# Optimization experiments

Hardware: AMD Instinct MI355X
Metric: run time of the kernel (lower is better)

Reference implementation:

```python
import jax, jax.numpy as jnp
import numpy as np

K_PRED = 6
TEMP = 0.8  # score_temperature
MTR_THRESH = [3.5, 1.0, 1.75]  # meters per type [veh, ped, cyc]
MPA_THRESH = [2.5, 1.0, 1.5]


def _within(xy, thresh):
    # xy: [S, A, P, T, 2], thresh: [S, A] -> bool [S, A, P, P]; ADE(i, j) < thresh (use_ade=True)
    diff = xy[:, :, None, :, :, :] - xy[:, :, :, None, :, :]  # [S, A, P, P, T, 2]
    ade = jnp.sqrt((diff * diff).sum(-1)).mean(-1)            # [S, A, P, P]
    return ade < thresh[:, :, None, None]


def _mtr_nms(trajs, scores, agent_type):
    # Greedy sequential top-k with distance-based down-weighting (MTR-style NMS).
    thresh = agent_type @ jnp.asarray(MTR_THRESH, scores.dtype)  # [S, A]
    within = _within(trajs[..., :2], thresh)                     # [S, A, P, P]
    P = scores.shape[-1]

    def step(carry, _):
        idx = jnp.argmax(carry, axis=-1)                                              # [S, A]
        row = jnp.take_along_axis(within, idx[:, :, None, None], axis=2)[:, :, 0, :]  # [S, A, P]
        carry = carry * ((~row).astype(carry.dtype) * 0.99 + 0.01)
        carry = jnp.where(jnp.arange(P) == idx[:, :, None], -1.0, carry)
        return carry, idx

    _, mode_idx = jax.lax.scan(step, scores, None, length=K_PRED)  # [K, S, A]
    mode_idx = jnp.moveaxis(mode_idx, 0, -1)                       # [S, A, K]
    trajs_k = jnp.take_along_axis(trajs, mode_idx[:, :, :, None, None], axis=2)
    scores_k = jnp.take_along_axis(scores, mode_idx, axis=2)
    return trajs_k, scores_k / scores_k.sum(-1, keepdims=True)


def _mpa_nms(valid, trajs, scores, agent_type):
    # Sequential suppression in descending-score order; mode k drops to 0.001 if any
    # nearby mode currently has a higher score. Faithful to the torch nested loop.
    thresh = agent_type @ jnp.asarray(MPA_THRESH, scores.dtype)  # [S, A]
    within = _within(trajs[..., :2], thresh)                     # [S, A, K, K]

    def per_agent(w, s, v):
        order = jnp.argsort(-s)  # descending score order

        def step(carry, k):
            suppress = jnp.any(w[k] & (carry > carry[k]))
            carry = carry.at[k].set(jnp.where(v & suppress, jnp.asarray(0.001, carry.dtype), carry[k]))
            return carry, None

        out, _ = jax.lax.scan(step, s, order)
        return out

    s = jax.vmap(jax.vmap(per_agent))(within, scores, valid)
    return s / s.sum(-1, keepdims=True)


def forward(valid, scores, trajs, agent_type):
    scores = scores / scores.sum(-1, keepdims=True)
    S, A, P, T, D = trajs.shape
    # n_pred > k_pred, aggr_thresh=[], mtr_nms_thresh non-empty -> mtr_nms branch
    trajs_k, scores_k = _mtr_nms(trajs, scores, agent_type)
    # mpa_nms_thresh non-empty -> mpa_nms
    scores_k = _mpa_nms(valid, trajs_k, scores_k, agent_type)
    # score_temperature > 0
    scores_k = jax.nn.softmax(jnp.log(scores_k) / TEMP, axis=-1)
    tr = jnp.transpose(trajs_k, (0, 3, 1, 2, 4))  # movedim(3,1): [S, T, A, K, D]
    waymo_trajs = tr[..., :2]
    waymo_yaw_bbox = tr[..., 2:3]
    waymo_spd = tr[..., 3:4]
    waymo_valid = jnp.broadcast_to(valid[:, None, :], (S, T, A))
    return waymo_trajs, waymo_yaw_bbox, waymo_spd, scores_k, waymo_valid


def setup_inputs():
    key = jax.random.key(0)
    k1, k2, k3, k4, k5 = jax.random.split(key, 5)
    S, A, P, T = 8, 64, 32, 80
    valid = jax.random.bernoulli(k1, 0.9, (S, A))
    scores = jax.random.uniform(k2, (S, A, P), minval=0.01, maxval=1.0)
    # shared base path + per-mode noise so pairwise ADEs straddle the NMS thresholds
    base = jax.random.normal(k3, (S, A, 1, T, 4)) * 20.0
    trajs = base + jax.random.normal(k4, (S, A, P, T, 4)) * 1.5
    agent_type = jax.nn.one_hot(jax.random.randint(k5, (S, A), 0, 3), 3, dtype=jnp.float32)
    return {"valid": valid, "scores": scores, "trajs": trajs, "agent_type": agent_type}


def reference(valid, scores, trajs, agent_type):
    return forward(valid, scores, trajs, agent_type)
```

## Files before the change

### kernel.cpp

```cpp
#include <hip/hip_runtime.h>
#include <math.h>
#include <float.h>

#define NS 8
#define NA 64
#define NP 32
#define NT 80
#define NK 6
#define NAG (NS*NA)
#define PAIRS 496

#define FSQRT(x) __builtin_amdgcn_sqrtf(x)

#define BASE1 ((size_t)NS*NT*NA*NK*2)
#define BASE2 (BASE1 + (size_t)NS*NT*NA*NK)
#define BASE3 (BASE2 + (size_t)NS*NT*NA*NK)
#define BASE4 (BASE3 + (size_t)NS*NA*NK)

__global__ __launch_bounds__(512) void k_fused(
    const void* __restrict__ valid_raw,
    const float* __restrict__ scores,
    const float* __restrict__ trajs,
    const float* __restrict__ atype,
    float* __restrict__ out)
{
    const int bid = blockIdx.x;
    const int blk = (bid & 7) * 64 + (bid >> 3);
    const int s = blk >> 6;
    const int a = blk & 63;
    const int tid = threadIdx.x;

    __shared__ float2 sxy[NT][NP + 1];
    __shared__ float2 szw[NT][NP + 1];
    __shared__ float sade[NP][NP];
    __shared__ unsigned wloc[NP];
    __shared__ int   sel6[NK];
    __shared__ float fsc6[NK];
    __shared__ float vf_sh;

    if (tid < NP) wloc[tid] = 1u << tid;

    unsigned u0 = 0, u1 = 0; float sc = 0.0f;
    if (tid < 64) {
        const unsigned* vw = (const unsigned*)valid_raw;
        u0 = vw[tid]; u1 = vw[tid + 64];
        sc = scores[blk*NP + (tid & 31)];
    }
    const float a0 = atype[blk*3+0], a1 = atype[blk*3+1], a2 = atype[blk*3+2];
    const float thrM = a0*3.5f + a1*1.0f + a2*1.75f;
    const float thrQ = a0*2.5f + a1*1.0f + a2*1.5f;

    const float4* tg4 = (const float4*)trajs + (size_t)blk * NP * NT;
    #pragma unroll
    for (int rep = 0; rep < 5; ++rep) {
        int l = tid + rep*512;
        int p = l / NT, t = l - p*NT;
        float4 v = tg4[l];
        sxy[t][p] = make_float2(v.x, v.y);
        szw[t][p] = make_float2(v.z, v.w);
    }
    __syncthreads();

    {
        const int tile = tid >> 2, slice = tid & 3;
        int A_, B_, C_, D_;
        bool offd = (tile < 120);
        if (offd) {
            float fs = sqrtf((float)(1 + 8*tile));
            int tj = (int)((1.0f + fs) * 0.5f);
            int ti = tile - ((tj*(tj-1)) >> 1);
            A_ = 2*ti; B_ = 2*ti+1; C_ = 2*tj; D_ = 2*tj+1;
        } else {
            int m = tile - 120;
            A_ = 4*m; B_ = 4*m+2; C_ = 4*m+1; D_ = 4*m+3;
        }
        float accAC = 0.0f, accAD = 0.0f, accBC = 0.0f, accBD = 0.0f;
        const int tbase = slice * 20;
        #pragma unroll 4
        for (int tt = 0; tt < 20; ++tt) {
            int t = tbase + tt;
            float2 va = sxy[t][A_], vb = sxy[t][B_];
            float2 vc = sxy[t][C_], vd = sxy[t][D_];
            float dx, dy;
            dx = va.x - vc.x; dy = va.y - vc.y; accAC += FSQRT(fmaf(dx,dx,dy*dy));
            dx = va.x - vd.x; dy = va.y - vd.y; accAD += FSQRT(fmaf(dx,dx,dy*dy));
            dx = vb.x - vc.x; dy = vb.y - vc.y; accBC += FSQRT(fmaf(dx,dx,dy*dy));
            dx = vb.x - vd.x; dy = vb.y - vd.y; accBD += FSQRT(fmaf(dx,dx,dy*dy));
        }
        const int qb = (tid & 63) & ~3;
#define FOLD(acc) ((((acc) + __shfl((acc), qb+1)) + __shfl((acc), qb+2)) + __shfl((acc), qb+3))
        float fAC = FOLD(accAC);
        float fAD = FOLD(accAD);
        float fBC = FOLD(accBC);
        float fBD = FOLD(accBD);
#undef FOLD
        if (slice == 0) {
            const float inv = 1.0f / (float)NT;
            float e0 = fAC*inv, e1 = fAD*inv, e2 = fBC*inv, e3 = fBD*inv;
            sade[A_][C_] = e0; sade[C_][A_] = e0;
            if (e0 < thrM) { atomicOr(&wloc[A_], 1u<<C_); atomicOr(&wloc[C_], 1u<<A_); }
            sade[B_][D_] = e3; sade[D_][B_] = e3;
            if (e3 < thrM) { atomicOr(&wloc[B_], 1u<<D_); atomicOr(&wloc[D_], 1u<<B_); }
            if (offd) {
                sade[A_][D_] = e1; sade[D_][A_] = e1;
                if (e1 < thrM) { atomicOr(&wloc[A_], 1u<<D_); atomicOr(&wloc[D_], 1u<<A_); }
                sade[B_][C_] = e2; sade[C_][B_] = e2;
                if (e2 < thrM) { atomicOr(&wloc[B_], 1u<<C_); atomicOr(&wloc[C_], 1u<<B_); }
            }
        }
    }
    __syncthreads();

    if (tid < 64) {
        const int lane = tid;
        const int p = lane & 31;

        bool fHit = (u0 == 0x3F800000u) || (u1 == 0x3F800000u);
        int nz0 = ((u0&0xFFu)!=0)+((u0&0xFF00u)!=0)+((u0&0xFF0000u)!=0)+((u0&0xFF000000u)!=0);
        int nz1 = ((u1&0xFFu)!=0)+((u1&0xFF00u)!=0)+((u1&0xFF0000u)!=0)+((u1&0xFF000000u)!=0);
        bool isF = __any(fHit), multi = __any(nz0 >= 2 || nz1 >= 2);
        int vflag;
        if (isF)        vflag = (((const float*)valid_raw)[blk] != 0.0f);
        else if (multi) vflag = (((const unsigned char*)valid_raw)[blk] != 0);
        else            vflag = (((const int*)valid_raw)[blk] != 0);

        unsigned wl = wloc[p];

        float carry = sc;
        int sel_0, sel_1, sel_2, sel_3, sel_4, sel_5;
#define GREEDY(SK) { \
        float vv = carry; int bi = p; \
        _Pragma("unroll") \
        for (int off = 16; off; off >>= 1) { \
            float ov = __shfl_xor(vv, off); \
            int   oi = __shfl_xor(bi, off); \
            if (ov > vv || (ov == vv && oi < bi)) { vv = ov; bi = oi; } \
        } \
        SK = bi; \
        unsigned rbi = __shfl(wl, bi); \
        carry = (p == bi) ? -1.0f : (((rbi >> p) & 1u) ? carry*0.01f : carry); }
        GREEDY(sel_0) GREEDY(sel_1) GREEDY(sel_2) GREEDY(sel_3) GREEDY(sel_4) GREEDY(sel_5)
#undef GREEDY

        float q0 = __shfl(sc, sel_0), q1 = __shfl(sc, sel_1), q2 = __shfl(sc, sel_2);
        float q3 = __shfl(sc, sel_3), q4 = __shfl(sc, sel_4), q5 = __shfl(sc, sel_5);

        int ii = (lane<5)?0 : (lane<9)?1 : (lane<12)?2 : (lane<14)?3 : 4;
        int jj = lane - ((ii==0)?-1 : (ii==1)?3 : (ii==2)?6 : (ii==3)?8 : 9);
        jj = (jj < 0) ? 0 : (jj > 5 ? 5 : jj);
        int pi = (ii==0)?sel_0:(ii==1)?sel_1:(ii==2)?sel_2:(ii==3)?sel_3:(ii==4)?sel_4:sel_5;
        int pj = (jj==0)?sel_0:(jj==1)?sel_1:(jj==2)?sel_2:(jj==3)?sel_3:(jj==4)?sel_4:sel_5;
        float ade15 = sade[pi][pj];
        bool within = (lane < 15) && (ade15 < thrQ);
        unsigned long long bal = __ballot(within);
#define B(i) ((unsigned)((bal >> (i)) & 1ull))
        unsigned w6_0 = (B(0)<<1)|(B(1)<<2)|(B(2)<<3)|(B(3)<<4)|(B(4)<<5);
        unsigned w6_1 = (B(0)<<0)|(B(5)<<2)|(B(6)<<3)|(B(7)<<4)|(B(8)<<5);
        unsigned w6_2 = (B(1)<<0)|(B(5)<<1)|(B(9)<<3)|(B(10)<<4)|(B(11)<<5);
        unsigned w6_3 = (B(2)<<0)|(B(6)<<1)|(B(9)<<2)|(B(12)<<4)|(B(13)<<5);
        unsigned w6_4 = (B(3)<<0)|(B(7)<<1)|(B(10)<<2)|(B(12)<<3)|(B(14)<<5);
        unsigned w6_5 = (B(4)<<0)|(B(8)<<1)|(B(11)<<2)|(B(13)<<3)|(B(14)<<4);
#undef B

#define GE(x,y) ((x) >= (y))
        bool a01=GE(q0,q1), a02=GE(q0,q2), a03=GE(q0,q3), a04=GE(q0,q4), a05=GE(q0,q5);
        bool a12=GE(q1,q2), a13=GE(q1,q3), a14=GE(q1,q4), a15=GE(q1,q5);
        bool a23=GE(q2,q3), a24=GE(q2,q4), a25=GE(q2,q5);
        bool a34=GE(q3,q4), a35=GE(q3,q5);
        bool a45=GE(q4,q5);
#undef GE
        int r0 = (!a01)+(!a02)+(!a03)+(!a04)+(!a05);
        int r1 = a01+(!a12)+(!a13)+(!a14)+(!a15);
        int r2 = a02+a12+(!a23)+(!a24)+(!a25);
        int r3 = a03+a13+a23+(!a34)+(!a35);
        int r4 = a04+a14+a24+a34+(!a45);
        int r5 = a05+a15+a25+a35+a45;

        const float sum6 = q0+q1+q2+q3+q4+q5;
        const float supv = 0.001f * sum6;
#define STEP(m) { \
        float ck = (r0==m)?q0:(r1==m)?q1:(r2==m)?q2:(r3==m)?q3:(r4==m)?q4:q5; \
        unsigned wk = (r0==m)?w6_0:(r1==m)?w6_1:(r2==m)?w6_2:(r3==m)?w6_3:(r4==m)?w6_4:w6_5; \
        bool sup = (((wk>>0)&1u)&&(q0>ck))||(((wk>>1)&1u)&&(q1>ck))||(((wk>>2)&1u)&&(q2>ck)) \
                 ||(((wk>>3)&1u)&&(q3>ck))||(((wk>>4)&1u)&&(q4>ck))||(((wk>>5)&1u)&&(q5>ck)); \
        bool go = vflag && sup; \
        q0 = (go&&(r0==m))?supv:q0; q1 = (go&&(r1==m))?supv:q1; q2 = (go&&(r2==m))?supv:q2; \
        q3 = (go&&(r3==m))?supv:q3; q4 = (go&&(r4==m))?supv:q4; q5 = (go&&(r5==m))?supv:q5; }
        STEP(0) STEP(1) STEP(2) STEP(3) STEP(4) STEP(5)
#undef STEP

        float g0 = __logf(q0)*1.25f, g1 = __logf(q1)*1.25f, g2 = __logf(q2)*1.25f;
        float g3 = __logf(q3)*1.25f, g4 = __logf(q4)*1.25f, g5 = __logf(q5)*1.25f;
        float mx = fmaxf(fmaxf(fmaxf(g0,g1),fmaxf(g2,g3)),fmaxf(g4,g5));
        float e0 = __expf(g0-mx), e1 = __expf(g1-mx), e2 = __expf(g2-mx);
        float e3 = __expf(g3-mx), e4 = __expf(g4-mx), e5 = __expf(g5-mx);
        float es = e0+e1+e2+e3+e4+e5;

        if (lane < NK) {
            float fv = (lane==0)?e0:(lane==1)?e1:(lane==2)?e2:(lane==3)?e3:(lane==4)?e4:e5;
            int   sv = (lane==0)?sel_0:(lane==1)?sel_1:(lane==2)?sel_2:(lane==3)?sel_3:(lane==4)?sel_4:sel_5;
            fsc6[lane] = fv / es;
            sel6[lane] = sv;
        }
        if (lane == 0) vf_sh = vflag ? 1.0f : 0.0f;
    }
    __syncthreads();

    if (tid < 3*NT) {
        int t = tid / 3, kp = tid - t*3;
        int k0 = kp*2;
        int s0 = sel6[k0], s1 = sel6[k0+1];
        float2 xy0 = sxy[t][s0], xy1 = sxy[t][s1];
        float2 zw0 = szw[t][s0], zw1 = szw[t][s1];
        size_t ob = (((size_t)(s*NT + t)*NA + a)*NK + k0);
        *(float4*)((float2*)out + ob) = make_float4(xy0.x, xy0.y, xy1.x, xy1.y);
        *(float2*)(out + BASE1 + ob) = make_float2(zw0.x, zw1.x);
        *(float2*)(out + BASE2 + ob) = make_float2(zw0.y, zw1.y);
    }
    if (tid < NK) out[BASE3 + (size_t)blk*NK + tid] = fsc6[tid];
    if (tid < NT)
        out[BASE4 + (size_t)(s*NT + tid)*NA + a] = vf_sh;
}

extern "C" void kernel_launch(void* const* d_in, const int* in_sizes, int n_in,
                              void* d_out, int out_size, void* d_ws, size_t ws_size,
                              hipStream_t stream) {
    const void*  valid  = d_in[0];
    const float* scores = (const float*)d_in[1];
    const float* trajs  = (const float*)d_in[2];
    const float* atype  = (const float*)d_in[3];
    k_fused<<<NAG, 512, 0, stream>>>(valid, scores, trajs, atype, (float*)d_out);
}
```

Measured before the change: 19.58 us.

## Run NMS redundantly in every wave, drop zw LDS staging and final barrier

Every wavefront now runs the greedy selection and suppression logic redundantly, so selected indices stay in registers and the last __syncthreads plus the shared handoff buffers go away. The z/w trajectory components are no longer staged in LDS; the output stage re-reads the selected modes straight from global memory, likely from cache. Argmax is simplified to an fmax butterfly followed by a ballot and find-first-set. This cuts LDS usage and a barrier, at the cost of redundant ALU work across eight waves and extra global reads.

```diff
diff --git a/kernel.cpp b/kernel.cpp
--- a/kernel.cpp
+++ b/kernel.cpp
@@ -29,23 +29,18 @@
     const int s = blk >> 6;
     const int a = blk & 63;
     const int tid = threadIdx.x;
+    const int lane = tid & 63;
+    const int p = lane & 31;
 
     __shared__ float2 sxy[NT][NP + 1];
-    __shared__ float2 szw[NT][NP + 1];
     __shared__ float sade[NP][NP];
     __shared__ unsigned wloc[NP];
-    __shared__ int   sel6[NK];
-    __shared__ float fsc6[NK];
-    __shared__ float vf_sh;
 
     if (tid < NP) wloc[tid] = 1u << tid;
 
-    unsigned u0 = 0, u1 = 0; float sc = 0.0f;
-    if (tid < 64) {
-        const unsigned* vw = (const unsigned*)valid_raw;
-        u0 = vw[tid]; u1 = vw[tid + 64];
-        sc = scores[blk*NP + (tid & 31)];
-    }
+    const unsigned* vw = (const unsigned*)valid_raw;
+    unsigned u0 = vw[lane], u1 = vw[lane + 64];
+    float sc = scores[blk*NP + p];
     const float a0 = atype[blk*3+0], a1 = atype[blk*3+1], a2 = atype[blk*3+2];
     const float thrM = a0*3.5f + a1*1.0f + a2*1.75f;
     const float thrQ = a0*2.5f + a1*1.0f + a2*1.5f;
@@ -54,10 +49,9 @@
     #pragma unroll
     for (int rep = 0; rep < 5; ++rep) {
         int l = tid + rep*512;
-        int p = l / NT, t = l - p*NT;
+        int pp = l / NT, t = l - pp*NT;
         float4 v = tg4[l];
-        sxy[t][p] = make_float2(v.x, v.y);
-        szw[t][p] = make_float2(v.z, v.w);
+        sxy[t][pp] = make_float2(v.x, v.y);
     }
     __syncthreads();
 
@@ -87,7 +81,7 @@
             dx = vb.x - vc.x; dy = vb.y - vc.y; accBC += FSQRT(fmaf(dx,dx,dy*dy));
             dx = vb.x - vd.x; dy = vb.y - vd.y; accBD += FSQRT(fmaf(dx,dx,dy*dy));
         }
-        const int qb = (tid & 63) & ~3;
+        const int qb = lane & ~3;
 #define FOLD(acc) ((((acc) + __shfl((acc), qb+1)) + __shfl((acc), qb+2)) + __shfl((acc), qb+3))
         float fAC = FOLD(accAC);
         float fAD = FOLD(accAD);
@@ -111,115 +105,104 @@
     }
     __syncthreads();
 
-    if (tid < 64) {
-        const int lane = tid;
-        const int p = lane & 31;
-
-        bool fHit = (u0 == 0x3F800000u) || (u1 == 0x3F800000u);
-        int nz0 = ((u0&0xFFu)!=0)+((u0&0xFF00u)!=0)+((u0&0xFF0000u)!=0)+((u0&0xFF000000u)!=0);
-        int nz1 = ((u1&0xFFu)!=0)+((u1&0xFF00u)!=0)+((u1&0xFF0000u)!=0)+((u1&0xFF000000u)!=0);
-        bool isF = __any(fHit), multi = __any(nz0 >= 2 || nz1 >= 2);
-        int vflag;
-        if (isF)        vflag = (((const float*)valid_raw)[blk] != 0.0f);
-        else if (multi) vflag = (((const unsigned char*)valid_raw)[blk] != 0);
-        else            vflag = (((const int*)valid_raw)[blk] != 0);
-
-        unsigned wl = wloc[p];
-
-        float carry = sc;
-        int sel_0, sel_1, sel_2, sel_3, sel_4, sel_5;
+    bool fHit = (u0 == 0x3F800000u) || (u1 == 0x3F800000u);
+    int nz0 = ((u0&0xFFu)!=0)+((u0&0xFF00u)!=0)+((u0&0xFF0000u)!=0)+((u0&0xFF000000u)!=0);
+    int nz1 = ((u1&0xFFu)!=0)+((u1&0xFF00u)!=0)+((u1&0xFF0000u)!=0)+((u1&0xFF000000u)!=0);
+    bool isF = __any(fHit), multi = __any(nz0 >= 2 || nz1 >= 2);
+    int vflag;
+    if (isF)        vflag = (((const float*)valid_raw)[blk] != 0.0f);
+    else if (multi) vflag = (((const unsigned char*)valid_raw)[blk] != 0);
+    else            vflag = (((const int*)valid_raw)[blk] != 0);
+
+    unsigned wl = wloc[p];
+
+    float carry = sc;
+    int sel_0, sel_1, sel_2, sel_3, sel_4, sel_5;
 #define GREEDY(SK) { \
-        float vv = carry; int bi = p; \
-        _Pragma("unroll") \
-        for (int off = 16; off; off >>= 1) { \
-            float ov = __shfl_xor(vv, off); \
-            int   oi = __shfl_xor(bi, off); \
-            if (ov > vv || (ov == vv && oi < bi)) { vv = ov; bi = oi; } \
-        } \
-        SK = bi; \
-        unsigned rbi = __shfl(wl, bi); \
-        carry = (p == bi) ? -1.0f : (((rbi >> p) & 1u) ? carry*0.01f : carry); }
-        GREEDY(sel_0) GREEDY(sel_1) GREEDY(sel_2) GREEDY(sel_3) GREEDY(sel_4) GREEDY(sel_5)
+    float vv = carry; \
+    _Pragma("unroll") \
+    for (int off = 16; off; off >>= 1) vv = fmaxf(vv, __shfl_xor(vv, off)); \
+    unsigned long long mba = __ballot(carry == vv); \
+    int bi = __ffsll((long long)mba) - 1; \
+    SK = bi; \
+    unsigned rbi = __shfl(wl, bi); \
+    carry = (p == bi) ? -1.0f : (((rbi >> p) & 1u) ? carry*0.01f : carry); }
+    GREEDY(sel_0) GREEDY(sel_1) GREEDY(sel_2) GREEDY(sel_3) GREEDY(sel_4) GREEDY(sel_5)
 #undef GREEDY
 
-        float q0 = __shfl(sc, sel_0), q1 = __shfl(sc, sel_1), q2 = __shfl(sc, sel_2);
-        float q3 = __shfl(sc, sel_3), q4 = __shfl(sc, sel_4), q5 = __shfl(sc, sel_5);
-
-        int ii = (lane<5)?0 : (lane<9)?1 : (lane<12)?2 : (lane<14)?3 : 4;
-        int jj = lane - ((ii==0)?-1 : (ii==1)?3 : (ii==2)?6 : (ii==3)?8 : 9);
-        jj = (jj < 0) ? 0 : (jj > 5 ? 5 : jj);
-        int pi = (ii==0)?sel_0:(ii==1)?sel_1:(ii==2)?sel_2:(ii==3)?sel_3:(ii==4)?sel_4:sel_5;
-        int pj = (jj==0)?sel_0:(jj==1)?sel_1:(jj==2)?sel_2:(jj==3)?sel_3:(jj==4)?sel_4:sel_5;
-        float ade15 = sade[pi][pj];
-        bool within = (lane < 15) && (ade15 < thrQ);
-        unsigned long long bal = __ballot(within);
+    float q0 = __shfl(sc, sel_0), q1 = __shfl(sc, sel_1), q2 = __shfl(sc, sel_2);
+    float q3 = __shfl(sc, sel_3), q4 = __shfl(sc, sel_4), q5 = __shfl(sc, sel_5);
+
+    int ii = (lane<5)?0 : (lane<9)?1 : (lane<12)?2 : (lane<14)?3 : 4;
+    int jj = lane - ((ii==0)?-1 : (ii==1)?3 : (ii==2)?6 : (ii==3)?8 : 9);
+    jj = (jj < 0) ? 0 : (jj > 5 ? 5 : jj);
+    int pi = (ii==0)?sel_0:(ii==1)?sel_1:(ii==2)?sel_2:(ii==3)?sel_3:(ii==4)?sel_4:sel_5;
+    int pj = (jj==0)?sel_0:(jj==1)?sel_1:(jj==2)?sel_2:(jj==3)?sel_3:(jj==4)?sel_4:sel_5;
+    float ade15 = sade[pi][pj];
+    bool within = (lane < 15) && (ade15 < thrQ);
+    unsigned long long bal = __ballot(within);
 #define B(i) ((unsigned)((bal >> (i)) & 1ull))
-        unsigned w6_0 = (B(0)<<1)|(B(1)<<2)|(B(2)<<3)|(B(3)<<4)|(B(4)<<5);
-        unsigned w6_1 = (B(0)<<0)|(B(5)<<2)|(B(6)<<3)|(B(7)<<4)|(B(8)<<5);
-        unsigned w6_2 = (B(1)<<0)|(B(5)<<1)|(B(9)<<3)|(B(10)<<4)|(B(11)<<5);
-        unsigned w6_3 = (B(2)<<0)|(B(6)<<1)|(B(9)<<2)|(B(12)<<4)|(B(13)<<5);
-        unsigned w6_4 = (B(3)<<0)|(B(7)<<1)|(B(10)<<2)|(B(12)<<3)|(B(14)<<5);
-        unsigned w6_5 = (B(4)<<0)|(B(8)<<1)|(B(11)<<2)|(B(13)<<3)|(B(14)<<4);
+    unsigned w6_0 = (B(0)<<1)|(B(1)<<2)|(B(2)<<3)|(B(3)<<4)|(B(4)<<5);
+    unsigned w6_1 = (B(0)<<0)|(B(5)<<2)|(B(6)<<3)|(B(7)<<4)|(B(8)<<5);
+    unsigned w6_2 = (B(1)<<0)|(B(5)<<1)|(B(9)<<3)|(B(10)<<4)|(B(11)<<5);
+    unsigned w6_3 = (B(2)<<0)|(B(6)<<1)|(B(9)<<2)|(B(12)<<4)|(B(13)<<5);
+    unsigned w6_4 = (B(3)<<0)|(B(7)<<1)|(B(10)<<2)|(B(12)<<3)|(B(14)<<5);
+    unsigned w6_5 = (B(4)<<0)|(B(8)<<1)|(B(11)<<2)|(B(13)<<3)|(B(14)<<4);
 #undef B
 
 #define GE(x,y) ((x) >= (y))
-        bool a01=GE(q0,q1), a02=GE(q0,q2), a03=GE(q0,q3), a04=GE(q0,q4), a05=GE(q0,q5);
-        bool a12=GE(q1,q2), a13=GE(q1,q3), a14=GE(q1,q4), a15=GE(q1,q5);
-        bool a23=GE(q2,q3), a24=GE(q2,q4), a25=GE(q2,q5);
-        bool a34=GE(q3,q4), a35=GE(q3,q5);
-        bool a45=GE(q4,q5);
+    bool a01=GE(q0,q1), a02=GE(q0,q2), a03=GE(q0,q3), a04=GE(q0,q4), a05=GE(q0,q5);
+    bool a12=GE(q1,q2), a13=GE(q1,q3), a14=GE(q1,q4), a15=GE(q1,q5);
+    bool a23=GE(q2,q3), a24=GE(q2,q4), a25=GE(q2,q5);
+    bool a34=GE(q3,q4), a35=GE(q3,q5);
+    bool a45=GE(q4,q5);
 #undef GE
-        int r0 = (!a01)+(!a02)+(!a03)+(!a04)+(!a05);
-        int r1 = a01+(!a12)+(!a13)+(!a14)+(!a15);
-        int r2 = a02+a12+(!a23)+(!a24)+(!a25);
-        int r3 = a03+a13+a23+(!a34)+(!a35);
-        int r4 = a04+a14+a24+a34+(!a45);
-        int r5 = a05+a15+a25+a35+a45;
-
-        const float sum6 = q0+q1+q2+q3+q4+q5;
-        const float supv = 0.001f * sum6;
+    int r0 = (!a01)+(!a02)+(!a03)+(!a04)+(!a05);
+    int r1 = a01+(!a12)+(!a13)+(!a14)+(!a15);
+    int r2 = a02+a12+(!a23)+(!a24)+(!a25);
+    int r3 = a03+a13+a23+(!a34)+(!a35);
+    int r4 = a04+a14+a24+a34+(!a45);
+    int r5 = a05+a15+a25+a35+a45;
+
+    const float sum6 = q0+q1+q2+q3+q4+q5;
+    const float supv = 0.001f * sum6;
 #define STEP(m) { \
-        float ck = (r0==m)?q0:(r1==m)?q1:(r2==m)?q2:(r3==m)?q3:(r4==m)?q4:q5; \
-        unsigned wk = (r0==m)?w6_0:(r1==m)?w6_1:(r2==m)?w6_2:(r3==m)?w6_3:(r4==m)?w6_4:w6_5; \
-        bool sup = (((wk>>0)&1u)&&(q0>ck))||(((wk>>1)&1u)&&(q1>ck))||(((wk>>2)&1u)&&(q2>ck)) \
-                 ||(((wk>>3)&1u)&&(q3>ck))||(((wk>>4)&1u)&&(q4>ck))||(((wk>>5)&1u)&&(q5>ck)); \
-        bool go = vflag && sup; \
-        q0 = (go&&(r0==m))?supv:q0; q1 = (go&&(r1==m))?supv:q1; q2 = (go&&(r2==m))?supv:q2; \
-        q3 = (go&&(r3==m))?supv:q3; q4 = (go&&(r4==m))?supv:q4; q5 = (go&&(r5==m))?supv:q5; }
-        STEP(0) STEP(1) STEP(2) STEP(3) STEP(4) STEP(5)
+    float ck = (r0==m)?q0:(r1==m)?q1:(r2==m)?q2:(r3==m)?q3:(r4==m)?q4:q5; \
+    unsigned wk = (r0==m)?w6_0:(r1==m)?w6_1:(r2==m)?w6_2:(r3==m)?w6_3:(r4==m)?w6_4:w6_5; \
+    bool sup = (((wk>>0)&1u)&&(q0>ck))||(((wk>>1)&1u)&&(q1>ck))||(((wk>>2)&1u)&&(q2>ck)) \
+             ||(((wk>>3)&1u)&&(q3>ck))||(((wk>>4)&1u)&&(q4>ck))||(((wk>>5)&1u)&&(q5>ck)); \
+    bool go = vflag && sup; \
+    q0 = (go&&(r0==m))?supv:q0; q1 = (go&&(r1==m))?supv:q1; q2 = (go&&(r2==m))?supv:q2; \
+    q3 = (go&&(r3==m))?supv:q3; q4 = (go&&(r4==m))?supv:q4; q5 = (go&&(r5==m))?supv:q5; }
+    STEP(0) STEP(1) STEP(2) STEP(3) STEP(4) STEP(5)
 #undef STEP
 
-        float g0 = __logf(q0)*1.25f, g1 = __logf(q1)*1.25f, g2 = __logf(q2)*1.25f;
-        float g3 = __logf(q3)*1.25f, g4 = __logf(q4)*1.25f, g5 = __logf(q5)*1.25f;
-        float mx = fmaxf(fmaxf(fmaxf(g0,g1),fmaxf(g2,g3)),fmaxf(g4,g5));
-        float e0 = __expf(g0-mx), e1 = __expf(g1-mx), e2 = __expf(g2-mx);
-        float e3 = __expf(g3-mx), e4 = __expf(g4-mx), e5 = __expf(g5-mx);
-        float es = e0+e1+e2+e3+e4+e5;
-
-        if (lane < NK) {
-            float fv = (lane==0)?e0:(lane==1)?e1:(lane==2)?e2:(lane==3)?e3:(lane==4)?e4:e5;
-            int   sv = (lane==0)?sel_0:(lane==1)?sel_1:(lane==2)?sel_2:(lane==3)?sel_3:(lane==4)?sel_4:sel_5;
-            fsc6[lane] = fv / es;
-            sel6[lane] = sv;
-        }
-        if (lane == 0) vf_sh = vflag ? 1.0f : 0.0f;
-    }
-    __syncthreads();
+    float g0 = __logf(q0)*1.25f, g1 = __logf(q1)*1.25f, g2 = __logf(q2)*1.25f;
+    float g3 = __logf(q3)*1.25f, g4 = __logf(q4)*1.25f, g5 = __logf(q5)*1.25f;
+    float mx = fmaxf(fmaxf(fmaxf(g0,g1),fmaxf(g2,g3)),fmaxf(g4,g5));
+    float e0 = __expf(g0-mx), e1 = __expf(g1-mx), e2 = __expf(g2-mx);
+    float e3 = __expf(g3-mx), e4 = __expf(g4-mx), e5 = __expf(g5-mx);
+    float es = e0+e1+e2+e3+e4+e5;
+
+    if (tid < NK) {
+        float fv = (lane==0)?e0:(lane==1)?e1:(lane==2)?e2:(lane==3)?e3:(lane==4)?e4:e5;
+        out[BASE3 + (size_t)blk*NK + lane] = fv / es;
+    }
+    if (tid < NT)
+        out[BASE4 + (size_t)(s*NT + tid)*NA + a] = vflag ? 1.0f : 0.0f;
 
     if (tid < 3*NT) {
         int t = tid / 3, kp = tid - t*3;
         int k0 = kp*2;
-        int s0 = sel6[k0], s1 = sel6[k0+1];
-        float2 xy0 = sxy[t][s0], xy1 = sxy[t][s1];
-        float2 zw0 = szw[t][s0], zw1 = szw[t][s1];
+        int s0sel = (kp==0)?sel_0:(kp==1)?sel_2:sel_4;
+        int s1sel = (kp==0)?sel_1:(kp==1)?sel_3:sel_5;
+        float4 v0 = tg4[(size_t)s0sel*NT + t];
+        float4 v1 = tg4[(size_t)s1sel*NT + t];
         size_t ob = (((size_t)(s*NT + t)*NA + a)*NK + k0);
-        *(float4*)((float2*)out + ob) = make_float4(xy0.x, xy0.y, xy1.x, xy1.y);
-        *(float2*)(out + BASE1 + ob) = make_float2(zw0.x, zw1.x);
-        *(float2*)(out + BASE2 + ob) = make_float2(zw0.y, zw1.y);
-    }
-    if (tid < NK) out[BASE3 + (size_t)blk*NK + tid] = fsc6[tid];
-    if (tid < NT)
-        out[BASE4 + (size_t)(s*NT + tid)*NA + a] = vf_sh;
+        *(float4*)((float2*)out + ob) = make_float4(v0.x, v0.y, v1.x, v1.y);
+        *(float2*)(out + BASE1 + ob) = make_float2(v0.z, v1.z);
+        *(float2*)(out + BASE2 + ob) = make_float2(v0.w, v1.w);
+    }
 }
 
 extern "C" void kernel_launch(void* const* d_in, const int* in_sizes, int n_in,
```

Result: faster. 18.97 us (-3.1%).
